# Kernel tuning notes

Measured on AMD Instinct MI355X. Metric: run time of the kernel, lower is better.

## Reference

```python
import jax, jax.numpy as jnp
import numpy as np

B, H, W, K, A = 4096, 32, 32, 20, 4


def setup_inputs() -> dict:
    key = jax.random.key(0)
    k_wall, k_agent, k_goal, k_phi, k_l1, k_l2 = jax.random.split(key, 6)
    # obs channels: 0 = wall/feature map (random), 1 = one-hot agent pos, 2 = one-hot goal pos
    walls = jax.random.uniform(k_wall, (B, H, W), dtype=jnp.float32)
    agent_idx = jax.random.randint(k_agent, (B,), 0, H * W)
    goal_idx = jax.random.randint(k_goal, (B,), 0, H * W)
    agent = jax.nn.one_hot(agent_idx, H * W, dtype=jnp.float32).reshape(B, H, W)
    goal = jax.nn.one_hot(goal_idx, H * W, dtype=jnp.float32).reshape(B, H, W)
    obs = jnp.stack([walls, agent, goal], axis=-1)  # (B,H,W,3)
    obs_flat = obs.reshape(B, H * W * 3)
    din = H * W * 3
    return {
        "obs_flat": obs_flat,
        "Phi_w": jax.random.normal(k_phi, (din, 2 * H * W), dtype=jnp.float32) * 0.02,
        "Phi_b": jnp.zeros((2 * H * W,), jnp.float32),
        "L1_w": jax.random.normal(k_l1, (36, 16), dtype=jnp.float32) * 0.1,
        "L1_b": jnp.zeros((16,), jnp.float32),
        "L2_w": jax.random.normal(k_l2, (16, A), dtype=jnp.float32) * 0.1,
        "L2_b": jnp.zeros((A,), jnp.float32),
    }


def _mvprop(r, p):
    # K-step value propagation: V <- max(V, r + p*(best 4-neighbor V - r))
    # p = sigmoid(...) >= 0, so max over the 4 shifted nv values equals nv of the max shift.
    def body(V, _):
        pv = jnp.pad(V, ((0, 0), (1, 1), (1, 1)))
        nbr = jnp.maximum(
            jnp.maximum(pv[:, :-2, 1:-1], pv[:, 2:, 1:-1]),   # up, down
            jnp.maximum(pv[:, 1:-1, :-2], pv[:, 1:-1, 2:]),   # left, right
        )
        return jnp.maximum(V, r + p * (nbr - r)), None
    V, _ = jax.lax.scan(body, r, None, length=K)
    return V


def reference(obs_flat, Phi_w, Phi_b, L1_w, L1_b, L2_w, L2_b):
    b = obs_flat.shape[0]
    obs = obs_flat.reshape(b, H, W, 3)
    phi = jax.nn.sigmoid(obs_flat @ Phi_w + Phi_b).reshape(b, H, W, 2)
    r, p = phi[..., 0], phi[..., 1]
    V = _mvprop(r, p)  # (b,H,W)
    obs_val = jnp.concatenate([obs, V[..., None]], axis=-1)  # (b,H,W,4)
    padded = jnp.pad(obs_val, ((0, 0), (1, 1), (1, 1), (0, 0)))
    # agent position: exactly one nonzero in channel 1 per sample -> argmax
    idx = jnp.argmax(obs[..., 1].reshape(b, -1), axis=1)
    pi, pj = idx // W, idx % W
    # 3x3 neighborhood around agent in padded grid (start = pos+1-1 = pos)
    def slice_one(ov, i, j):
        return jax.lax.dynamic_slice(ov, (i, j, 0), (3, 3, 4))
    sel = jax.vmap(slice_one)(padded, pi, pj)  # (b,3,3,4)
    h = jax.nn.relu(sel.reshape(b, 36) @ L1_w + L1_b)
    logit = h @ L2_w + L2_b
    return logit
```

## Files before the change

kernel.cpp:

```cpp
#include <hip/hip_runtime.h>
#include <hip/hip_fp16.h>

#define BATCH 4096
#define HH 32
#define WW 32
#define KPROP 20
#define NACT 4
#define DIN 3072
#define DPHI 2048
#define HWC 1024
#define KC 1024

typedef _Float16 h8_t __attribute__((ext_vector_type(8)));
typedef _Float16 h4_t __attribute__((ext_vector_type(4)));
typedef float f32x4 __attribute__((ext_vector_type(4)));

__device__ inline void load_lds16(const _Float16* g, _Float16* l) {
    __builtin_amdgcn_global_load_lds(
        (const __attribute__((address_space(1))) void*)g,
        (__attribute__((address_space(3))) void*)l, 16, 0, 0);
}

__device__ inline float sigmoidf(float x) { return 1.0f / (1.0f + __expf(-x)); }

__device__ inline float dpp_shr1(float x) {
    return __int_as_float(__builtin_amdgcn_update_dpp(
        0, __float_as_int(x), 0x111, 0xF, 0xF, true));
}
__device__ inline float dpp_shl1(float x) {
    return __int_as_float(__builtin_amdgcn_update_dpp(
        0, __float_as_int(x), 0x101, 0xF, 0xF, true));
}

__global__ __launch_bounds__(256) void prep_kernel(
    const float* __restrict__ obs,
    _Float16* __restrict__ W16,
    int* __restrict__ aidx, int* __restrict__ gidx)
{
    const int t = blockIdx.x * 256 + threadIdx.x;
    const int b = t >> 8;
    const int c0 = (t & 255) * 4;
    const float* src = obs + (size_t)b * DIN + 3 * c0;
    const float4 f0 = *(const float4*)(src);
    const float4 f1 = *(const float4*)(src + 4);
    const float4 f2 = *(const float4*)(src + 8);
    h4_t w;
    w[0] = (_Float16)f0.x; w[1] = (_Float16)f0.w;
    w[2] = (_Float16)f1.z; w[3] = (_Float16)f2.y;
    *(h4_t*)(W16 + (size_t)b * KC + c0) = w;
    if (f0.y > 0.5f) aidx[b] = c0;
    if (f1.x > 0.5f) aidx[b] = c0 + 1;
    if (f1.w > 0.5f) aidx[b] = c0 + 2;
    if (f2.z > 0.5f) aidx[b] = c0 + 3;
    if (f0.z > 0.5f) gidx[b] = c0;
    if (f1.y > 0.5f) gidx[b] = c0 + 1;
    if (f2.x > 0.5f) gidx[b] = c0 + 2;
    if (f2.w > 0.5f) gidx[b] = c0 + 3;
}

__global__ __launch_bounds__(256) void wprep_kernel(
    const float* __restrict__ Phi_w,
    _Float16* __restrict__ PwT,
    _Float16* __restrict__ Pag)
{
    __shared__ float tile[32][33];
    const int tx = threadIdx.x & 31;
    const int ty = threadIdx.x >> 5;
    const int ci = blockIdx.y;
    const int ni = blockIdx.x;
    #pragma unroll
    for (int s = 0; s < 4; s++) {
        const int r = ty + 8 * s;
        const int c = ci * 32 + r;
        const int n = ni * 32 + tx;
        tile[r][tx] = Phi_w[(size_t)(3 * c) * DPHI + n];
        Pag[(size_t)c * DPHI + n]                      = (_Float16)Phi_w[(size_t)(3 * c + 1) * DPHI + n];
        Pag[(size_t)(HWC + c) * DPHI + n]              = (_Float16)Phi_w[(size_t)(3 * c + 2) * DPHI + n];
    }
    __syncthreads();
    #pragma unroll
    for (int s = 0; s < 4; s++) {
        const int r = ty + 8 * s;
        PwT[(size_t)(ni * 32 + r) * KC + ci * 32 + tx] = (_Float16)tile[tx][r];
    }
}

#define BM 128
#define BN 128

__device__ inline void stage_tile(const _Float16* Abase, const _Float16* Bbase, int k0,
                                  _Float16* As, _Float16* Bs, int tid) {
    const int sk0 = tid >> 7;
    #pragma unroll
    for (int r2 = 0; r2 < 2; r2++) {
        const int kqs = sk0 + 2 * r2;
        load_lds16(Abase + k0 + kqs * 8, As + (tid + 256 * r2) * 8);
        load_lds16(Bbase + k0 + kqs * 8, Bs + (tid + 256 * r2) * 8);
    }
}

__global__ __launch_bounds__(256) void gemm_pre_kernel(
    const _Float16* __restrict__ A,
    const _Float16* __restrict__ Bt,
    const float* __restrict__ bias,
    _Float16* __restrict__ pre)
{
    __shared__ _Float16 As[2][4 * BM * 8];
    __shared__ _Float16 Bs[2][4 * BN * 8];

    const int tid  = threadIdx.x;
    const int lane = tid & 63;
    const int wid  = tid >> 6;
    const int m0 = blockIdx.y * BM;
    const int n0 = blockIdx.x * BN;
    const int wm = (wid >> 1) * 64;
    const int wn = (wid & 1) * 64;
    const int lm = lane & 15;
    const int kq = lane >> 4;

    f32x4 acc[4][4] = {};

    const int sm = tid & 127;
    const _Float16* Abase = A  + (size_t)(m0 + sm) * KC;
    const _Float16* Bbase = Bt + (size_t)(n0 + sm) * KC;

    stage_tile(Abase, Bbase, 0, As[0], Bs[0], tid);

    int cur = 0;
    for (int k0 = 0; k0 < KC; k0 += 32) {
        __syncthreads();
        if (k0 + 32 < KC)
            stage_tile(Abase, Bbase, k0 + 32, As[cur ^ 1], Bs[cur ^ 1], tid);

        h8_t af[4], bf[4];
        #pragma unroll
        for (int mt = 0; mt < 4; mt++)
            af[mt] = *(const h8_t*)(As[cur] + (kq * BM + wm + mt * 16 + lm) * 8);
        #pragma unroll
        for (int nt = 0; nt < 4; nt++)
            bf[nt] = *(const h8_t*)(Bs[cur] + (kq * BN + wn + nt * 16 + lm) * 8);

        #pragma unroll
        for (int mt = 0; mt < 4; mt++)
            #pragma unroll
            for (int nt = 0; nt < 4; nt++)
                acc[mt][nt] = __builtin_amdgcn_mfma_f32_16x16x32_f16(
                    af[mt], bf[nt], acc[mt][nt], 0, 0, 0);
        cur ^= 1;
    }

    #pragma unroll
    for (int nt = 0; nt < 4; nt++) {
        const int col = n0 + wn + nt * 16 + lm;
        const float bcol = bias[col];
        #pragma unroll
        for (int mt = 0; mt < 4; mt++) {
            #pragma unroll
            for (int r = 0; r < 4; r++) {
                const int row = m0 + wm + mt * 16 + kq * 4 + r;
                pre[(size_t)row * DPHI + col] = (_Float16)(acc[mt][nt][r] + bcol);
            }
        }
    }
}

__global__ __launch_bounds__(256, 4) void vprop_head_kernel(
    const _Float16* __restrict__ pre,
    const _Float16* __restrict__ Pag,
    const float* __restrict__ obs,
    const int* __restrict__ aidx,
    const int* __restrict__ gidx,
    const float* __restrict__ L1w,
    const float* __restrict__ L1b,
    const float* __restrict__ L2w,
    const float* __restrict__ L2b,
    float* __restrict__ out)
{
    __shared__ __align__(16) float Vg[4][HWC];
    __shared__ float sel[4][36], hbuf[4][16];

    const int tid  = threadIdx.x;
    const int w    = tid >> 6;
    const int lane = tid & 63;
    const int b    = blockIdx.x * 4 + w;
    const int bi   = lane & 15;
    const int bj   = lane >> 4;
    const int ai = aidx[b];
    const int gi = gidx[b];

    const _Float16* pb = pre + (size_t)b * DPHI;
    const _Float16* ra = Pag + (size_t)ai * DPHI;
    const _Float16* rg = Pag + (size_t)(HWC + gi) * DPHI;

    float v[2][8], p[2][8], a[2][8];
    #pragma unroll
    for (int r = 0; r < 2; r++) {
        const int off = 64 * (2 * bi + r) + 16 * bj;
        const h8_t ph0 = *(const h8_t*)(pb + off), ph1 = *(const h8_t*)(pb + off + 8);
        const h8_t pa0 = *(const h8_t*)(ra + off), pa1 = *(const h8_t*)(ra + off + 8);
        const h8_t pg0 = *(const h8_t*)(rg + off), pg1 = *(const h8_t*)(rg + off + 8);
        #pragma unroll
        for (int c = 0; c < 4; c++) {
            const float rv = sigmoidf((float)ph0[2*c]   + (float)pa0[2*c]   + (float)pg0[2*c]);
            const float pv = sigmoidf((float)ph0[2*c+1] + (float)pa0[2*c+1] + (float)pg0[2*c+1]);
            v[r][c] = rv; p[r][c] = pv; a[r][c] = rv * (1.0f - pv);
            const float rv2 = sigmoidf((float)ph1[2*c]   + (float)pa1[2*c]   + (float)pg1[2*c]);
            const float pv2 = sigmoidf((float)ph1[2*c+1] + (float)pa1[2*c+1] + (float)pg1[2*c+1]);
            v[r][c+4] = rv2; p[r][c+4] = pv2; a[r][c+4] = rv2 * (1.0f - pv2);
        }
    }

    for (int it = 0; it < KPROP; it++) {
        float uh[8], dh[8], lh[2], rh[2];
        #pragma unroll
        for (int c = 0; c < 8; c++) {
            uh[c] = dpp_shr1(v[1][c]);
            dh[c] = dpp_shl1(v[0][c]);
        }
        #pragma unroll
        for (int r = 0; r < 2; r++) {
            lh[r] = __shfl(v[r][7], lane - 16);
            rh[r] = __shfl(v[r][0], lane + 16);
            if (bj == 0) lh[r] = 0.0f;
            if (bj == 3) rh[r] = 0.0f;
        }
        float nb[2][8];
        #pragma unroll
        for (int c = 0; c < 8; c++) {
            const float lf0 = (c == 0) ? lh[0] : v[0][c-1];
            const float rt0 = (c == 7) ? rh[0] : v[0][c+1];
            const float lf1 = (c == 0) ? lh[1] : v[1][c-1];
            const float rt1 = (c == 7) ? rh[1] : v[1][c+1];
            nb[0][c] = fmaxf(fmaxf(uh[c], v[1][c]), fmaxf(lf0, rt0));
            nb[1][c] = fmaxf(fmaxf(v[0][c], dh[c]), fmaxf(lf1, rt1));
        }
        #pragma unroll
        for (int r = 0; r < 2; r++)
            #pragma unroll
            for (int c = 0; c < 8; c++)
                v[r][c] = fmaxf(v[r][c], fmaf(p[r][c], nb[r][c], a[r][c]));
    }

    #pragma unroll
    for (int r = 0; r < 2; r++) {
        float4 lo, hi;
        lo.x = v[r][0]; lo.y = v[r][1]; lo.z = v[r][2]; lo.w = v[r][3];
        hi.x = v[r][4]; hi.y = v[r][5]; hi.z = v[r][6]; hi.w = v[r][7];
        const int base = (2 * bi + r) * 32 + 8 * bj;
        *(float4*)&Vg[w][base]     = lo;
        *(float4*)&Vg[w][base + 4] = hi;
    }
    __syncthreads();

    const int pi = ai >> 5, pj = ai & 31;
    if (lane < 36) {
        const int cell = lane >> 2;
        const int ch = lane & 3;
        const int di = pi + cell / 3 - 1;
        const int dj = pj + cell % 3 - 1;
        float vv = 0.0f;
        if (di >= 0 && di < HH && dj >= 0 && dj < WW) {
            const int c = di * WW + dj;
            vv = (ch < 3) ? obs[(size_t)b * DIN + 3 * c + ch] : Vg[w][c];
        }
        sel[w][lane] = vv;
    }
    __syncthreads();

    if (lane < 16) {
        float h = L1b[lane];
        #pragma unroll
        for (int k = 0; k < 36; k++) h += sel[w][k] * L1w[k * 16 + lane];
        hbuf[w][lane] = fmaxf(h, 0.0f);
    }
    __syncthreads();

    if (lane < 4) {
        float o = L2b[lane];
        #pragma unroll
        for (int t = 0; t < 16; t++) o += hbuf[w][t] * L2w[t * 4 + lane];
        out[(size_t)b * NACT + lane] = o;
    }
}

extern "C" void kernel_launch(void* const* d_in, const int* in_sizes, int n_in,
                              void* d_out, int out_size, void* d_ws, size_t ws_size,
                              hipStream_t stream) {
    const float* obs   = (const float*)d_in[0];
    const float* Phi_w = (const float*)d_in[1];
    const float* Phi_b = (const float*)d_in[2];
    const float* L1w   = (const float*)d_in[3];
    const float* L1b   = (const float*)d_in[4];
    const float* L2w   = (const float*)d_in[5];
    const float* L2b   = (const float*)d_in[6];
    float* out = (float*)d_out;

    char* ws = (char*)d_ws;
    _Float16* pre = (_Float16*)ws;
    _Float16* W16 = (_Float16*)(ws + 16777216);
    _Float16* PwT = (_Float16*)(ws + 25165824);
    _Float16* Pag = (_Float16*)(ws + 29360128);
    int* aidx = (int*)(ws + 37748736);
    int* gidx = aidx + BATCH;

    prep_kernel<<<BATCH, 256, 0, stream>>>(obs, W16, aidx, gidx);
    wprep_kernel<<<dim3(64, 32), 256, 0, stream>>>(Phi_w, PwT, Pag);
    gemm_pre_kernel<<<dim3(DPHI / BN, BATCH / BM), 256, 0, stream>>>(W16, PwT, Phi_b, pre);
    vprop_head_kernel<<<BATCH / 4, 256, 0, stream>>>(pre, Pag, obs, aidx, gidx,
                                                     L1w, L1b, L2w, L2b, out);
}
```

Baseline: 178.5 us.

## Merge input and weight prep kernels; shrink GEMM M-tile to 64 rows

Folds the observation prep and Phi weight transpose/convert kernels into one launch, selecting the role by block index, to cut a kernel launch and let both jobs overlap on the device. The GEMM block tile drops from 128x128 to 64x128 with a matching launch-bounds hint, doubling the block count and halving per-wave accumulators so more blocks can be resident at once. In exchange each block reuses its B tile across fewer rows, so more B data is loaded from memory and staged through LDS overall.

```diff
diff --git a/kernel.cpp b/kernel.cpp
--- a/kernel.cpp
+++ b/kernel.cpp
@@ -32,74 +32,74 @@
         0, __float_as_int(x), 0x101, 0xF, 0xF, true));
 }
 
-__global__ __launch_bounds__(256) void prep_kernel(
+__global__ __launch_bounds__(256) void prep_fused_kernel(
     const float* __restrict__ obs,
+    const float* __restrict__ Phi_w,
     _Float16* __restrict__ W16,
+    _Float16* __restrict__ PwT,
+    _Float16* __restrict__ Pag,
     int* __restrict__ aidx, int* __restrict__ gidx)
 {
-    const int t = blockIdx.x * 256 + threadIdx.x;
-    const int b = t >> 8;
-    const int c0 = (t & 255) * 4;
-    const float* src = obs + (size_t)b * DIN + 3 * c0;
-    const float4 f0 = *(const float4*)(src);
-    const float4 f1 = *(const float4*)(src + 4);
-    const float4 f2 = *(const float4*)(src + 8);
-    h4_t w;
-    w[0] = (_Float16)f0.x; w[1] = (_Float16)f0.w;
-    w[2] = (_Float16)f1.z; w[3] = (_Float16)f2.y;
-    *(h4_t*)(W16 + (size_t)b * KC + c0) = w;
-    if (f0.y > 0.5f) aidx[b] = c0;
-    if (f1.x > 0.5f) aidx[b] = c0 + 1;
-    if (f1.w > 0.5f) aidx[b] = c0 + 2;
-    if (f2.z > 0.5f) aidx[b] = c0 + 3;
-    if (f0.z > 0.5f) gidx[b] = c0;
-    if (f1.y > 0.5f) gidx[b] = c0 + 1;
-    if (f2.x > 0.5f) gidx[b] = c0 + 2;
-    if (f2.w > 0.5f) gidx[b] = c0 + 3;
-}
-
-__global__ __launch_bounds__(256) void wprep_kernel(
-    const float* __restrict__ Phi_w,
-    _Float16* __restrict__ PwT,
-    _Float16* __restrict__ Pag)
-{
     __shared__ float tile[32][33];
-    const int tx = threadIdx.x & 31;
-    const int ty = threadIdx.x >> 5;
-    const int ci = blockIdx.y;
-    const int ni = blockIdx.x;
-    #pragma unroll
-    for (int s = 0; s < 4; s++) {
-        const int r = ty + 8 * s;
-        const int c = ci * 32 + r;
-        const int n = ni * 32 + tx;
-        tile[r][tx] = Phi_w[(size_t)(3 * c) * DPHI + n];
-        Pag[(size_t)c * DPHI + n]                      = (_Float16)Phi_w[(size_t)(3 * c + 1) * DPHI + n];
-        Pag[(size_t)(HWC + c) * DPHI + n]              = (_Float16)Phi_w[(size_t)(3 * c + 2) * DPHI + n];
-    }
-    __syncthreads();
-    #pragma unroll
-    for (int s = 0; s < 4; s++) {
-        const int r = ty + 8 * s;
-        PwT[(size_t)(ni * 32 + r) * KC + ci * 32 + tx] = (_Float16)tile[tx][r];
-    }
-}
-
-#define BM 128
+    if (blockIdx.x < BATCH) {
+        const int t = blockIdx.x * 256 + threadIdx.x;
+        const int b = t >> 8;
+        const int c0 = (t & 255) * 4;
+        const float* src = obs + (size_t)b * DIN + 3 * c0;
+        const float4 f0 = *(const float4*)(src);
+        const float4 f1 = *(const float4*)(src + 4);
+        const float4 f2 = *(const float4*)(src + 8);
+        h4_t w;
+        w[0] = (_Float16)f0.x; w[1] = (_Float16)f0.w;
+        w[2] = (_Float16)f1.z; w[3] = (_Float16)f2.y;
+        *(h4_t*)(W16 + (size_t)b * KC + c0) = w;
+        if (f0.y > 0.5f) aidx[b] = c0;
+        if (f1.x > 0.5f) aidx[b] = c0 + 1;
+        if (f1.w > 0.5f) aidx[b] = c0 + 2;
+        if (f2.z > 0.5f) aidx[b] = c0 + 3;
+        if (f0.z > 0.5f) gidx[b] = c0;
+        if (f1.y > 0.5f) gidx[b] = c0 + 1;
+        if (f2.x > 0.5f) gidx[b] = c0 + 2;
+        if (f2.w > 0.5f) gidx[b] = c0 + 3;
+    } else {
+        const int bid = blockIdx.x - BATCH;
+        const int ni = bid & 63;
+        const int ci = bid >> 6;
+        const int tx = threadIdx.x & 31;
+        const int ty = threadIdx.x >> 5;
+        #pragma unroll
+        for (int s = 0; s < 4; s++) {
+            const int r = ty + 8 * s;
+            const int c = ci * 32 + r;
+            const int n = ni * 32 + tx;
+            tile[r][tx] = Phi_w[(size_t)(3 * c) * DPHI + n];
+            Pag[(size_t)c * DPHI + n]         = (_Float16)Phi_w[(size_t)(3 * c + 1) * DPHI + n];
+            Pag[(size_t)(HWC + c) * DPHI + n] = (_Float16)Phi_w[(size_t)(3 * c + 2) * DPHI + n];
+        }
+        __syncthreads();
+        #pragma unroll
+        for (int s = 0; s < 4; s++) {
+            const int r = ty + 8 * s;
+            PwT[(size_t)(ni * 32 + r) * KC + ci * 32 + tx] = (_Float16)tile[tx][r];
+        }
+    }
+}
+
+#define BM 64
 #define BN 128
 
-__device__ inline void stage_tile(const _Float16* Abase, const _Float16* Bbase, int k0,
+__device__ inline void stage_tile(const _Float16* Arow, const _Float16* Bbase, int k0,
                                   _Float16* As, _Float16* Bs, int tid) {
+    load_lds16(Arow + k0, As + tid * 8);
     const int sk0 = tid >> 7;
     #pragma unroll
     for (int r2 = 0; r2 < 2; r2++) {
         const int kqs = sk0 + 2 * r2;
-        load_lds16(Abase + k0 + kqs * 8, As + (tid + 256 * r2) * 8);
         load_lds16(Bbase + k0 + kqs * 8, Bs + (tid + 256 * r2) * 8);
     }
 }
 
-__global__ __launch_bounds__(256) void gemm_pre_kernel(
+__global__ __launch_bounds__(256, 4) void gemm_pre_kernel(
     const _Float16* __restrict__ A,
     const _Float16* __restrict__ Bt,
     const float* __restrict__ bias,
@@ -113,35 +113,34 @@
     const int wid  = tid >> 6;
     const int m0 = blockIdx.y * BM;
     const int n0 = blockIdx.x * BN;
-    const int wm = (wid >> 1) * 64;
+    const int wm = (wid >> 1) * 32;
     const int wn = (wid & 1) * 64;
     const int lm = lane & 15;
     const int kq = lane >> 4;
 
-    f32x4 acc[4][4] = {};
-
-    const int sm = tid & 127;
-    const _Float16* Abase = A  + (size_t)(m0 + sm) * KC;
-    const _Float16* Bbase = Bt + (size_t)(n0 + sm) * KC;
-
-    stage_tile(Abase, Bbase, 0, As[0], Bs[0], tid);
+    f32x4 acc[2][4] = {};
+
+    const _Float16* Arow  = A  + (size_t)(m0 + (tid & 63)) * KC + (tid >> 6) * 8;
+    const _Float16* Bbase = Bt + (size_t)(n0 + (tid & 127)) * KC;
+
+    stage_tile(Arow, Bbase, 0, As[0], Bs[0], tid);
 
     int cur = 0;
     for (int k0 = 0; k0 < KC; k0 += 32) {
         __syncthreads();
         if (k0 + 32 < KC)
-            stage_tile(Abase, Bbase, k0 + 32, As[cur ^ 1], Bs[cur ^ 1], tid);
-
-        h8_t af[4], bf[4];
-        #pragma unroll
-        for (int mt = 0; mt < 4; mt++)
+            stage_tile(Arow, Bbase, k0 + 32, As[cur ^ 1], Bs[cur ^ 1], tid);
+
+        h8_t af[2], bf[4];
+        #pragma unroll
+        for (int mt = 0; mt < 2; mt++)
             af[mt] = *(const h8_t*)(As[cur] + (kq * BM + wm + mt * 16 + lm) * 8);
         #pragma unroll
         for (int nt = 0; nt < 4; nt++)
             bf[nt] = *(const h8_t*)(Bs[cur] + (kq * BN + wn + nt * 16 + lm) * 8);
 
         #pragma unroll
-        for (int mt = 0; mt < 4; mt++)
+        for (int mt = 0; mt < 2; mt++)
             #pragma unroll
             for (int nt = 0; nt < 4; nt++)
                 acc[mt][nt] = __builtin_amdgcn_mfma_f32_16x16x32_f16(
@@ -154,7 +153,7 @@
         const int col = n0 + wn + nt * 16 + lm;
         const float bcol = bias[col];
         #pragma unroll
-        for (int mt = 0; mt < 4; mt++) {
+        for (int mt = 0; mt < 2; mt++) {
             #pragma unroll
             for (int r = 0; r < 4; r++) {
                 const int row = m0 + wm + mt * 16 + kq * 4 + r;
@@ -303,8 +302,7 @@
     int* aidx = (int*)(ws + 37748736);
     int* gidx = aidx + BATCH;
 
-    prep_kernel<<<BATCH, 256, 0, stream>>>(obs, W16, aidx, gidx);
-    wprep_kernel<<<dim3(64, 32), 256, 0, stream>>>(Phi_w, PwT, Pag);
+    prep_fused_kernel<<<BATCH + 2048, 256, 0, stream>>>(obs, Phi_w, W16, PwT, Pag, aidx, gidx);
     gemm_pre_kernel<<<dim3(DPHI / BN, BATCH / BM), 256, 0, stream>>>(W16, PwT, Phi_b, pre);
     vprop_head_kernel<<<BATCH / 4, 256, 0, stream>>>(pre, Pag, obs, aidx, gidx,
                                                      L1w, L1b, L2w, L2b, out);
```

After: 185.5 us. 3.9% more time.
